# Performance work log

Hardware: AMD Instinct MI355X
Metric: run time of the kernel (lower is better)

Reference implementation:

```python
import jax, jax.numpy as jnp
import numpy as np

N_NODES = 50000
N_EDGES = 800000
N_GRAPHS = 128
IN_CH, HIDDEN, OUT_CH = 16, 64, 2


def gcn_conv(x, src, dst, W, b, n_nodes):
    """GCNConv: add self-loops, sym-normalized adjacency scatter-add, linear."""
    h = x @ W  # [N, H]
    loop = jnp.arange(n_nodes, dtype=src.dtype)
    s = jnp.concatenate([src, loop])  # [E+N]
    d = jnp.concatenate([dst, loop])
    deg = jax.ops.segment_sum(jnp.ones_like(d, dtype=h.dtype), d, num_segments=n_nodes)
    dinv = jnp.where(deg > 0, jax.lax.rsqrt(deg), 0.0)  # deg^{-1/2}
    norm = dinv[s] * dinv[d]  # [E+N]
    msg = h[s] * norm[:, None]  # gather + scale, [E+N, H]
    out = jax.ops.segment_sum(msg, d, num_segments=n_nodes)  # scatter-add
    return out + b


def global_mean_pool(x, batch, n_graphs):
    sums = jax.ops.segment_sum(x, batch, num_segments=n_graphs)
    cnts = jax.ops.segment_sum(jnp.ones((x.shape[0],), x.dtype), batch, num_segments=n_graphs)
    return sums / jnp.maximum(cnts, 1.0)[:, None]


def setup_inputs() -> dict:
    key = jax.random.key(0)
    ks = jax.random.split(key, 10)
    x = jax.random.normal(ks[0], (N_NODES, IN_CH), dtype=jnp.float32)
    edge_index = jax.random.randint(ks[1], (2, N_EDGES), 0, N_NODES, dtype=jnp.int64)
    batch = jnp.sort(jax.random.randint(ks[2], (N_NODES,), 0, N_GRAPHS, dtype=jnp.int64))
    def glorot(k, shp):
        lim = float(np.sqrt(6.0 / (shp[0] + shp[1])))
        return jax.random.uniform(k, shp, jnp.float32, -lim, lim)
    W1 = glorot(ks[3], (IN_CH, HIDDEN))
    b1 = jnp.zeros((HIDDEN,), jnp.float32)
    W2 = glorot(ks[4], (HIDDEN, HIDDEN))
    b2 = jnp.zeros((HIDDEN,), jnp.float32)
    Wc = glorot(ks[5], (HIDDEN, OUT_CH))
    bc = jnp.zeros((OUT_CH,), jnp.float32)
    return {"x": x, "edge_index": edge_index, "batch": batch,
            "W1": W1, "b1": b1, "W2": W2, "b2": b2, "Wc": Wc, "bc": bc}


def reference(x, edge_index, batch, W1, b1, W2, b2, Wc, bc):
    src, dst = edge_index[0], edge_index[1]
    n = x.shape[0]
    h = jax.nn.relu(gcn_conv(x, src, dst, W1, b1, n))
    # dropout p=0.3 is identity in eval mode
    h = jax.nn.relu(gcn_conv(h, src, dst, W2, b2, n))
    g = global_mean_pool(h, batch, N_GRAPHS)  # [G, H]
    return g @ Wc + bc  # [G, out_channels]
```

## Files before the change

kernel.cpp:

```cpp
#include <hip/hip_runtime.h>
#include <hip/hip_bf16.h>

#define N_NODES 50000
#define N_EDGES 800000
#define N_GRAPHS 128
#define IN_CH 16
#define HIDDEN 64
#define OUT_CH 2

#define BSHIFT 7
#define BNODES 128
#define NB ((N_NODES + BNODES - 1) / BNODES)
#define ECHUNK 4096
#define EB ((N_EDGES + ECHUNK - 1) / ECHUNK)
#define SLEN (NB * EB)
#define SCHUNK 1024
#define NSB ((SLEN + SCHUNK - 1) / SCHUNK)
#define MAXK 12
#define WT1_LD 18
#define AGG_LD 72
#define W2T_ENT (HIDDEN * AGG_LD)

typedef __attribute__((ext_vector_type(8))) short bf16x8;
typedef __attribute__((ext_vector_type(4))) float f32x4;

__device__ __forceinline__ float bf2f(unsigned short u) {
    return __uint_as_float(((unsigned)u) << 16);
}
__device__ __forceinline__ unsigned short f2bf(float f) {
    __hip_bfloat16 h = __float2bfloat16(f);
    return *reinterpret_cast<unsigned short*>(&h);
}


__global__ void bucket_hist_kernel(const int* __restrict__ dst, int* __restrict__ bh,
                                   float* __restrict__ sums, float* __restrict__ cntg,
                                   const float* __restrict__ W2, unsigned short* __restrict__ w2t) {
    __shared__ int lh[NB];
    int t = threadIdx.x;
    if (blockIdx.x == 0) {
        for (int i = t; i < N_GRAPHS * HIDDEN; i += 256) sums[i] = 0.0f;
        if (t < N_GRAPHS) cntg[t] = 0.0f;
    }
    if (blockIdx.x == 1) {
        for (int i = t; i < HIDDEN * HIDDEN; i += 256) {
            int k = i >> 6, c = i & 63;
            w2t[c * AGG_LD + k] = f2bf(W2[i]);
        }
    }
    for (int i = t; i < NB; i += 256) lh[i] = 0;
    __syncthreads();
    int base = blockIdx.x * ECHUNK;
    for (int i = t; i < ECHUNK; i += 256) {
        int e = base + i;
        if (e < N_EDGES) {
            int d = dst[e];
            if ((unsigned)d < N_NODES) atomicAdd(&lh[d >> BSHIFT], 1);
        }
    }
    __syncthreads();
    for (int i = t; i < NB; i += 256) bh[i * EB + blockIdx.x] = lh[i];
}

__global__ void scan_part_kernel(const int* __restrict__ a, int* __restrict__ bsum) {
    __shared__ int s[256];
    int t = threadIdx.x;
    int ebase = blockIdx.x * SCHUNK + t * 4;
    int v = 0;
    if (ebase + 3 < SLEN) {
        int4 c = *(const int4*)&a[ebase];
        v = c.x + c.y + c.z + c.w;
    } else {
        for (int k = 0; k < 4; k++) {
            int i = ebase + k;
            if (i < SLEN) v += a[i];
        }
    }
    s[t] = v;
    __syncthreads();
    for (int off = 128; off > 0; off >>= 1) {
        if (t < off) s[t] += s[t + off];
        __syncthreads();
    }
    if (t == 0) bsum[blockIdx.x] = s[0];
}

__global__ void scan_apply_kernel(const int* __restrict__ a, const int* __restrict__ bsum,
                                  int* __restrict__ boff) {
    __shared__ int sb[256];
    __shared__ int st[256];
    int t = threadIdx.x;
    sb[t] = (t < NSB) ? bsum[t] : 0;
    __syncthreads();
    for (int off = 1; off < 256; off <<= 1) {
        int u = (t >= off) ? sb[t - off] : 0;
        __syncthreads();
        sb[t] += u;
        __syncthreads();
    }
    int blockOff = (blockIdx.x > 0) ? sb[blockIdx.x - 1] : 0;

    int ebase = blockIdx.x * SCHUNK + t * 4;
    int c0 = 0, c1 = 0, c2 = 0, c3 = 0;
    bool full = (ebase + 3 < SLEN);
    if (full) {
        int4 c = *(const int4*)&a[ebase];
        c0 = c.x; c1 = c.y; c2 = c.z; c3 = c.w;
    } else {
        if (ebase < SLEN) c0 = a[ebase];
        if (ebase + 1 < SLEN) c1 = a[ebase + 1];
        if (ebase + 2 < SLEN) c2 = a[ebase + 2];
    }
    int tsum = c0 + c1 + c2 + c3;
    st[t] = tsum;
    __syncthreads();
    for (int off = 1; off < 256; off <<= 1) {
        int u = (t >= off) ? st[t - off] : 0;
        __syncthreads();
        st[t] += u;
        __syncthreads();
    }
    int p = blockOff + st[t] - tsum;
    if (full) {
        int4 o;
        o.x = p; o.y = p + c0; o.z = p + c0 + c1; o.w = p + c0 + c1 + c2;
        *(int4*)&boff[ebase] = o;
    } else {
        if (ebase < SLEN) boff[ebase] = p;
        if (ebase + 1 < SLEN) boff[ebase + 1] = p + c0;
        if (ebase + 2 < SLEN) boff[ebase + 2] = p + c0 + c1;
        if (ebase + 3 < SLEN) boff[ebase + 3] = p + c0 + c1 + c2;
    }
}

__global__ void bucket_scatter_kernel(const int* __restrict__ src, const int* __restrict__ dst,
                                      const int* __restrict__ boff, int* __restrict__ pairs) {
    __shared__ int lcnt[NB];
    __shared__ int goff[NB];
    int t = threadIdx.x;
    for (int i = t; i < NB; i += 256) {
        lcnt[i] = 0;
        goff[i] = boff[i * EB + blockIdx.x];
    }
    __syncthreads();
    int base = blockIdx.x * ECHUNK;
    for (int i = t; i < ECHUNK; i += 256) {
        int e = base + i;
        if (e < N_EDGES) {
            int d = dst[e];
            if ((unsigned)d < N_NODES) {
                int b = d >> BSHIFT;
                int r = atomicAdd(&lcnt[b], 1);
                pairs[goff[b] + r] = (src[e] << BSHIFT) | (d & (BNODES - 1));
            }
        }
    }
}

__global__ void bucket_csr_kernel(const int* __restrict__ pairs, const int* __restrict__ boff,
                                  int* __restrict__ csr, int* __restrict__ rowptr,
                                  int* __restrict__ cnt_node, float* __restrict__ dinv) {
    __shared__ int lcnt[BNODES];
    __shared__ int ls[BNODES];
    __shared__ int lrow[BNODES];
    int b = blockIdx.x;
    int t = threadIdx.x;
    if (t < BNODES) lcnt[t] = 0;
    __syncthreads();
    int bstart = boff[b * EB];
    int bend = (b + 1 < NB) ? boff[(b + 1) * EB] : N_EDGES;
    int K = bend - bstart;
    int myp[MAXK], myr[MAXK];
#pragma unroll
    for (int k = 0; k < MAXK; k++) {
        int i = k * 256 + t;
        if (i < K) {
            int p = pairs[bstart + i];
            myp[k] = p;
            myr[k] = atomicAdd(&lcnt[p & (BNODES - 1)], 1);
        }
    }
    __syncthreads();
    if (t < BNODES) ls[t] = lcnt[t];
    __syncthreads();
    for (int off = 1; off < BNODES; off <<= 1) {
        int u = (t >= off && t < BNODES) ? ls[t - off] : 0;
        __syncthreads();
        if (t < BNODES) ls[t] += u;
        __syncthreads();
    }
    if (t < BNODES) {
        int ex = ls[t] - lcnt[t];
        lrow[t] = ex;
        int n = b * BNODES + t;
        if (n < N_NODES) {
            rowptr[n] = bstart + ex;
            cnt_node[n] = lcnt[t];
            dinv[n] = rsqrtf((float)(lcnt[t] + 1));
        }
    }
    __syncthreads();
#pragma unroll
    for (int k = 0; k < MAXK; k++) {
        int i = k * 256 + t;
        if (i < K) csr[bstart + lrow[myp[k] & (BNODES - 1)] + myr[k]] = myp[k] >> BSHIFT;
    }
}


__global__ void fused_l1_kernel(const float* __restrict__ x, const int* __restrict__ csr_src,
                                const int* __restrict__ rowptr, const int* __restrict__ cnt,
                                const float* __restrict__ dinv, const float* __restrict__ W,
                                const float* __restrict__ b, __hip_bfloat16* __restrict__ h) {
    __shared__ float sWT[HIDDEN * WT1_LD];
    __shared__ float sx[16 * IN_CH];
    int t = threadIdx.x;
    for (int i = t; i < IN_CH * HIDDEN; i += 256) {
        int k = i >> 6, c = i & 63;
        sWT[c * WT1_LD + k] = W[i];
    }

    int n0 = blockIdx.x * 16;
    int w = t >> 6;
    int lane = t & 63;
    int e16 = lane >> 2;
    int cc = (lane & 3) * 4;

    int lens[4], starts[4];
#pragma unroll
    for (int q = 0; q < 4; q++) {
        int n = n0 + w * 4 + q;
        lens[q] = cnt[n];
        starts[q] = rowptr[n];
    }

    for (int q = 0; q < 4; q++) {
        int row = w * 4 + q;
        int n = n0 + row;
        int len = lens[q];
        int start = starts[q];
        float4 acc = make_float4(0.f, 0.f, 0.f, 0.f);
        for (int i = e16; i < len; i += 16) {
            int s = csr_src[start + i];
            float dv = dinv[s];
            float4 xv = *(const float4*)&x[s * IN_CH + cc];
            acc.x += dv * xv.x; acc.y += dv * xv.y;
            acc.z += dv * xv.z; acc.w += dv * xv.w;
        }
#pragma unroll
        for (int m = 4; m <= 32; m <<= 1) {
            acc.x += __shfl_xor(acc.x, m, 64);
            acc.y += __shfl_xor(acc.y, m, 64);
            acc.z += __shfl_xor(acc.z, m, 64);
            acc.w += __shfl_xor(acc.w, m, 64);
        }
        if (lane < 4) {
            float dn = dinv[n];
            float4 xs = *(const float4*)&x[n * IN_CH + cc];
            float4 v;
            v.x = dn * acc.x + dn * dn * xs.x;
            v.y = dn * acc.y + dn * dn * xs.y;
            v.z = dn * acc.z + dn * dn * xs.z;
            v.w = dn * acc.w + dn * dn * xs.w;
            *(float4*)&sx[row * IN_CH + cc] = v;
        }
    }
    __syncthreads();

    int r = w;
    int c = t & 63;
    float bias = b[c];
#pragma unroll
    for (int nb = 0; nb < 4; nb++) {
        int row = nb * 4 + r;
        int n = n0 + row;
        if (n >= N_NODES) continue;
        float acch = bias;
#pragma unroll
        for (int k4 = 0; k4 < IN_CH; k4 += 4) {
            float4 a = *(const float4*)&sx[row * IN_CH + k4];
            float2 w0 = *(const float2*)&sWT[c * WT1_LD + k4];
            float2 w1 = *(const float2*)&sWT[c * WT1_LD + k4 + 2];
            acch += a.x * w0.x + a.y * w0.y + a.z * w1.x + a.w * w1.y;
        }
        float v = acch > 0.0f ? acch : 0.0f;
        h[n * HIDDEN + c] = __float2bfloat16(dinv[n] * v);
    }
}


__global__ void fused_l2_kernel(const __hip_bfloat16* __restrict__ h, const int* __restrict__ csr_src,
                                const int* __restrict__ rowptr, const int* __restrict__ cnt,
                                const float* __restrict__ dinv, const unsigned short* __restrict__ w2t,
                                const float* __restrict__ b, const int* __restrict__ batch,
                                float* __restrict__ sums, float* __restrict__ cntg) {
    __shared__ unsigned short sW[W2T_ENT];
    __shared__ unsigned short sagg[16 * AGG_LD];
    int t = threadIdx.x;
    {
        const uint4* wp = (const uint4*)w2t;
        uint4* sWv = (uint4*)sW;
#pragma unroll
        for (int i = 0; i < 3; i++) {
            int idx = i * 256 + t;
            if (idx < W2T_ENT / 8) sWv[idx] = wp[idx];
        }
    }

    int n0 = blockIdx.x * 16;
    int w = t >> 6;
    int lane = t & 63;
    int e4 = lane >> 4;
    int cc = (lane & 15) * 4;
    const unsigned short* hu = (const unsigned short*)h;

    int lens[4], starts[4];
#pragma unroll
    for (int q = 0; q < 4; q++) {
        int n = n0 + w * 4 + q;
        lens[q] = cnt[n];
        starts[q] = rowptr[n];
    }

    for (int q = 0; q < 4; q++) {
        int row = w * 4 + q;
        int n = n0 + row;
        int len = lens[q];
        int start = starts[q];
        float4 acc = make_float4(0.f, 0.f, 0.f, 0.f);
        int last = len - 1;
        int iters = (len + 15) >> 4;
        for (int m = 0; m < iters; m++) {
            int base = m * 16 + e4;
#pragma unroll
            for (int k = 0; k < 4; k++) {
                int j = base + 4 * k;
                int jj = j <= last ? j : last;
                float msk = j <= last ? 1.0f : 0.0f;
                int s = csr_src[start + jj];
                ushort4 a = *(const ushort4*)&hu[s * HIDDEN + cc];
                acc.x += msk * bf2f(a.x);
                acc.y += msk * bf2f(a.y);
                acc.z += msk * bf2f(a.z);
                acc.w += msk * bf2f(a.w);
            }
        }
        acc.x += __shfl_xor(acc.x, 16, 64);
        acc.y += __shfl_xor(acc.y, 16, 64);
        acc.z += __shfl_xor(acc.z, 16, 64);
        acc.w += __shfl_xor(acc.w, 16, 64);
        acc.x += __shfl_xor(acc.x, 32, 64);
        acc.y += __shfl_xor(acc.y, 32, 64);
        acc.z += __shfl_xor(acc.z, 32, 64);
        acc.w += __shfl_xor(acc.w, 32, 64);
        if (lane < 16) {
            ushort4 sv = *(const ushort4*)&hu[n * HIDDEN + cc];
            float dn = dinv[n];
            ushort4 o;
            o.x = f2bf(dn * (acc.x + bf2f(sv.x)));
            o.y = f2bf(dn * (acc.y + bf2f(sv.y)));
            o.z = f2bf(dn * (acc.z + bf2f(sv.z)));
            o.w = f2bf(dn * (acc.w + bf2f(sv.w)));
            *(ushort4*)&sagg[row * AGG_LD + cc] = o;
        }
    }
    __syncthreads();

    int quad = lane >> 4;
    int col = lane & 15;
    int cch = w * 16 + col;
    bf16x8 a0 = *(const bf16x8*)&sagg[col * AGG_LD + quad * 8];
    bf16x8 a1 = *(const bf16x8*)&sagg[col * AGG_LD + 32 + quad * 8];
    bf16x8 b0 = *(const bf16x8*)&sW[cch * AGG_LD + quad * 8];
    bf16x8 b1 = *(const bf16x8*)&sW[cch * AGG_LD + 32 + quad * 8];
    f32x4 d = {0.f, 0.f, 0.f, 0.f};
    d = __builtin_amdgcn_mfma_f32_16x16x32_bf16(a0, b0, d, 0, 0, 0);
    d = __builtin_amdgcn_mfma_f32_16x16x32_bf16(a1, b1, d, 0, 0, 0);
    float bias = b[cch];
    float v[4];
#pragma unroll
    for (int r = 0; r < 4; r++) {
        float z = d[r] + bias;
        v[r] = z > 0.0f ? z : 0.0f;
    }

    int glo = batch[n0];
    int ghi = batch[n0 + 15];
    if (glo == ghi) {
        float s4 = (v[0] + v[1]) + (v[2] + v[3]);
        s4 += __shfl_xor(s4, 16, 64);
        s4 += __shfl_xor(s4, 32, 64);
        if (quad == 0) atomicAdd(&sums[glo * HIDDEN + cch], s4);
        if (t == 0) atomicAdd(&cntg[glo], 16.0f);
    } else {
#pragma unroll
        for (int r = 0; r < 4; r++) {
            int g = batch[n0 + quad * 4 + r];
            if ((unsigned)g < N_GRAPHS) atomicAdd(&sums[g * HIDDEN + cch], v[r]);
        }
        if (w == 0 && col == 0) {
#pragma unroll
            for (int r = 0; r < 4; r++) {
                int g = batch[n0 + quad * 4 + r];
                if ((unsigned)g < N_GRAPHS) atomicAdd(&cntg[g], 1.0f);
            }
        }
    }
}


__global__ void head_kernel(const float* __restrict__ sums, const float* __restrict__ cntg,
                            const float* __restrict__ Wc, const float* __restrict__ bc,
                            float* __restrict__ out) {
    int t = blockIdx.x * blockDim.x + threadIdx.x;
    if (t >= N_GRAPHS * OUT_CH) return;
    int g = t >> 1;
    int o = t & 1;
    float inv = 1.0f / fmaxf(cntg[g], 1.0f);
    float acc = bc[o];
#pragma unroll
    for (int k = 0; k < HIDDEN; k++) acc += sums[g * HIDDEN + k] * inv * Wc[k * OUT_CH + o];
    out[t] = acc;
}


extern "C" void kernel_launch(void* const* d_in, const int* in_sizes, int n_in,
                              void* d_out, int out_size, void* d_ws, size_t ws_size,
                              hipStream_t stream) {
    const float* x  = (const float*)d_in[0];
    const int* ei   = (const int*)d_in[1];
    const int* bat  = (const int*)d_in[2];
    const float* W1 = (const float*)d_in[3];
    const float* b1 = (const float*)d_in[4];
    const float* W2 = (const float*)d_in[5];
    const float* b2 = (const float*)d_in[6];
    const float* Wc = (const float*)d_in[7];
    const float* bc = (const float*)d_in[8];
    float* out = (float*)d_out;

    const int* src = ei;
    const int* dst = ei + N_EDGES;

    char* ws = (char*)d_ws;
    size_t off = 0;
    auto carve = [&](size_t nbytes) {
        char* p = ws + off;
        off += (nbytes + 255) & ~(size_t)255;
        return p;
    };
    float* sums     = (float*)carve(N_GRAPHS * HIDDEN * sizeof(float));
    float* cntg     = (float*)carve(N_GRAPHS * sizeof(float));
    unsigned short* w2t = (unsigned short*)carve(W2T_ENT * sizeof(unsigned short));
    int*   bh       = (int*)carve((size_t)SLEN * sizeof(int));
    int*   bsum     = (int*)carve(NSB * sizeof(int));
    int*   boff     = (int*)carve((size_t)SLEN * sizeof(int));
    int*   pairs    = (int*)carve((size_t)N_EDGES * sizeof(int));
    int*   csr      = (int*)carve((size_t)N_EDGES * sizeof(int));
    int*   rowptr   = (int*)carve(N_NODES * sizeof(int));
    int*   cnt_node = (int*)carve(N_NODES * sizeof(int));
    float* dinv     = (float*)carve(N_NODES * sizeof(float));
    __hip_bfloat16* bufA = (__hip_bfloat16*)carve((size_t)N_NODES * HIDDEN * sizeof(__hip_bfloat16));
    (void)ws_size;

    const int node16Blk = (N_NODES + 15) / 16;

    bucket_hist_kernel<<<EB, 256, 0, stream>>>(dst, bh, sums, cntg, W2, w2t);
    scan_part_kernel<<<NSB, 256, 0, stream>>>(bh, bsum);
    scan_apply_kernel<<<NSB, 256, 0, stream>>>(bh, bsum, boff);
    bucket_scatter_kernel<<<EB, 256, 0, stream>>>(src, dst, boff, pairs);
    bucket_csr_kernel<<<NB, 256, 0, stream>>>(pairs, boff, csr, rowptr, cnt_node, dinv);

    fused_l1_kernel<<<node16Blk, 256, 0, stream>>>(x, csr, rowptr, cnt_node, dinv, W1, b1, bufA);
    fused_l2_kernel<<<node16Blk, 256, 0, stream>>>(bufA, csr, rowptr, cnt_node, dinv, w2t, b2,
                                                   bat, sums, cntg);
    head_kernel<<<1, 256, 0, stream>>>(sums, cntg, Wc, bc, out);
}
```

Measured before the change: 171.9 us.

## Replace scan-based bucketing with fixed-capacity atomic buckets and prescaled features

Drops the histogram and two scan kernels. Edges are now placed into fixed-capacity per-bucket slots (BCAP), with offsets claimed through global atomics in the scatter kernel. The CSR kernel also writes x prescaled by dinv, so layer 1 skips the per-edge dinv gather and unrolls its gather two-wide. Layer 2's gather switches to 8 bf16 per lane with 16-byte loads. Edges beyond BCAP in a bucket are silently dropped, and edge order within a bucket becomes nondeterministic.

```diff
diff --git a/kernel.cpp b/kernel.cpp
--- a/kernel.cpp
+++ b/kernel.cpp
@@ -11,11 +11,9 @@
 #define BSHIFT 7
 #define BNODES 128
 #define NB ((N_NODES + BNODES - 1) / BNODES)
+#define BCAP 3072
 #define ECHUNK 4096
 #define EB ((N_EDGES + ECHUNK - 1) / ECHUNK)
-#define SLEN (NB * EB)
-#define SCHUNK 1024
-#define NSB ((SLEN + SCHUNK - 1) / SCHUNK)
 #define MAXK 12
 #define WT1_LD 18
 #define AGG_LD 72
@@ -33,143 +31,69 @@
 }
 
 
-__global__ void bucket_hist_kernel(const int* __restrict__ dst, int* __restrict__ bh,
-                                   float* __restrict__ sums, float* __restrict__ cntg,
-                                   const float* __restrict__ W2, unsigned short* __restrict__ w2t) {
-    __shared__ int lh[NB];
+__global__ void init_kernel(int* __restrict__ zbase, int zwords,
+                            const float* __restrict__ W2, unsigned short* __restrict__ w2t) {
+    int gid = blockIdx.x * 256 + threadIdx.x;
+    int gsz = gridDim.x * 256;
+    for (int i = gid; i < zwords; i += gsz) zbase[i] = 0;
+    for (int i = gid; i < HIDDEN * HIDDEN; i += gsz) {
+        int k = i >> 6, c = i & 63;
+        w2t[c * AGG_LD + k] = f2bf(W2[i]);
+    }
+}
+
+
+__global__ void bucket_scatter_kernel(const int* __restrict__ src, const int* __restrict__ dst,
+                                      int* __restrict__ bcnt, int* __restrict__ pairs) {
+    __shared__ int lcnt[NB];
+    __shared__ int goff[NB];
+    __shared__ int lcur[NB];
     int t = threadIdx.x;
-    if (blockIdx.x == 0) {
-        for (int i = t; i < N_GRAPHS * HIDDEN; i += 256) sums[i] = 0.0f;
-        if (t < N_GRAPHS) cntg[t] = 0.0f;
-    }
-    if (blockIdx.x == 1) {
-        for (int i = t; i < HIDDEN * HIDDEN; i += 256) {
-            int k = i >> 6, c = i & 63;
-            w2t[c * AGG_LD + k] = f2bf(W2[i]);
-        }
-    }
-    for (int i = t; i < NB; i += 256) lh[i] = 0;
+    for (int i = t; i < NB; i += 256) lcnt[i] = 0;
     __syncthreads();
     int base = blockIdx.x * ECHUNK;
     for (int i = t; i < ECHUNK; i += 256) {
         int e = base + i;
         if (e < N_EDGES) {
             int d = dst[e];
-            if ((unsigned)d < N_NODES) atomicAdd(&lh[d >> BSHIFT], 1);
-        }
-    }
-    __syncthreads();
-    for (int i = t; i < NB; i += 256) bh[i * EB + blockIdx.x] = lh[i];
-}
-
-__global__ void scan_part_kernel(const int* __restrict__ a, int* __restrict__ bsum) {
-    __shared__ int s[256];
-    int t = threadIdx.x;
-    int ebase = blockIdx.x * SCHUNK + t * 4;
-    int v = 0;
-    if (ebase + 3 < SLEN) {
-        int4 c = *(const int4*)&a[ebase];
-        v = c.x + c.y + c.z + c.w;
-    } else {
-        for (int k = 0; k < 4; k++) {
-            int i = ebase + k;
-            if (i < SLEN) v += a[i];
-        }
-    }
-    s[t] = v;
-    __syncthreads();
-    for (int off = 128; off > 0; off >>= 1) {
-        if (t < off) s[t] += s[t + off];
-        __syncthreads();
-    }
-    if (t == 0) bsum[blockIdx.x] = s[0];
-}
-
-__global__ void scan_apply_kernel(const int* __restrict__ a, const int* __restrict__ bsum,
-                                  int* __restrict__ boff) {
-    __shared__ int sb[256];
-    __shared__ int st[256];
-    int t = threadIdx.x;
-    sb[t] = (t < NSB) ? bsum[t] : 0;
-    __syncthreads();
-    for (int off = 1; off < 256; off <<= 1) {
-        int u = (t >= off) ? sb[t - off] : 0;
-        __syncthreads();
-        sb[t] += u;
-        __syncthreads();
-    }
-    int blockOff = (blockIdx.x > 0) ? sb[blockIdx.x - 1] : 0;
-
-    int ebase = blockIdx.x * SCHUNK + t * 4;
-    int c0 = 0, c1 = 0, c2 = 0, c3 = 0;
-    bool full = (ebase + 3 < SLEN);
-    if (full) {
-        int4 c = *(const int4*)&a[ebase];
-        c0 = c.x; c1 = c.y; c2 = c.z; c3 = c.w;
-    } else {
-        if (ebase < SLEN) c0 = a[ebase];
-        if (ebase + 1 < SLEN) c1 = a[ebase + 1];
-        if (ebase + 2 < SLEN) c2 = a[ebase + 2];
-    }
-    int tsum = c0 + c1 + c2 + c3;
-    st[t] = tsum;
-    __syncthreads();
-    for (int off = 1; off < 256; off <<= 1) {
-        int u = (t >= off) ? st[t - off] : 0;
-        __syncthreads();
-        st[t] += u;
-        __syncthreads();
-    }
-    int p = blockOff + st[t] - tsum;
-    if (full) {
-        int4 o;
-        o.x = p; o.y = p + c0; o.z = p + c0 + c1; o.w = p + c0 + c1 + c2;
-        *(int4*)&boff[ebase] = o;
-    } else {
-        if (ebase < SLEN) boff[ebase] = p;
-        if (ebase + 1 < SLEN) boff[ebase + 1] = p + c0;
-        if (ebase + 2 < SLEN) boff[ebase + 2] = p + c0 + c1;
-        if (ebase + 3 < SLEN) boff[ebase + 3] = p + c0 + c1 + c2;
-    }
-}
-
-__global__ void bucket_scatter_kernel(const int* __restrict__ src, const int* __restrict__ dst,
-                                      const int* __restrict__ boff, int* __restrict__ pairs) {
-    __shared__ int lcnt[NB];
-    __shared__ int goff[NB];
-    int t = threadIdx.x;
+            if ((unsigned)d < N_NODES) atomicAdd(&lcnt[d >> BSHIFT], 1);
+        }
+    }
+    __syncthreads();
     for (int i = t; i < NB; i += 256) {
-        lcnt[i] = 0;
-        goff[i] = boff[i * EB + blockIdx.x];
-    }
-    __syncthreads();
-    int base = blockIdx.x * ECHUNK;
+        int c = lcnt[i];
+        goff[i] = (c > 0) ? atomicAdd(&bcnt[i], c) : 0;
+        lcur[i] = 0;
+    }
+    __syncthreads();
     for (int i = t; i < ECHUNK; i += 256) {
         int e = base + i;
         if (e < N_EDGES) {
             int d = dst[e];
             if ((unsigned)d < N_NODES) {
                 int b = d >> BSHIFT;
-                int r = atomicAdd(&lcnt[b], 1);
-                pairs[goff[b] + r] = (src[e] << BSHIFT) | (d & (BNODES - 1));
+                int r = goff[b] + atomicAdd(&lcur[b], 1);
+                if (r < BCAP) pairs[b * BCAP + r] = (src[e] << BSHIFT) | (d & (BNODES - 1));
             }
         }
     }
 }
 
-__global__ void bucket_csr_kernel(const int* __restrict__ pairs, const int* __restrict__ boff,
+__global__ void bucket_csr_kernel(const int* __restrict__ pairs, const int* __restrict__ bcnt,
                                   int* __restrict__ csr, int* __restrict__ rowptr,
-                                  int* __restrict__ cnt_node, float* __restrict__ dinv) {
+                                  int* __restrict__ cnt_node, float* __restrict__ dinv,
+                                  const float* __restrict__ x, float* __restrict__ xs) {
     __shared__ int lcnt[BNODES];
     __shared__ int ls[BNODES];
     __shared__ int lrow[BNODES];
+    __shared__ float sdv[BNODES];
     int b = blockIdx.x;
     int t = threadIdx.x;
     if (t < BNODES) lcnt[t] = 0;
     __syncthreads();
-    int bstart = boff[b * EB];
-    int bend = (b + 1 < NB) ? boff[(b + 1) * EB] : N_EDGES;
-    int K = bend - bstart;
+    int bstart = b * BCAP;
+    int K = bcnt[b];
+    if (K > BCAP) K = BCAP;
     int myp[MAXK], myr[MAXK];
 #pragma unroll
     for (int k = 0; k < MAXK; k++) {
@@ -192,11 +116,13 @@
     if (t < BNODES) {
         int ex = ls[t] - lcnt[t];
         lrow[t] = ex;
+        float dv = rsqrtf((float)(lcnt[t] + 1));
+        sdv[t] = dv;
         int n = b * BNODES + t;
         if (n < N_NODES) {
             rowptr[n] = bstart + ex;
             cnt_node[n] = lcnt[t];
-            dinv[n] = rsqrtf((float)(lcnt[t] + 1));
+            dinv[n] = dv;
         }
     }
     __syncthreads();
@@ -205,10 +131,15 @@
         int i = k * 256 + t;
         if (i < K) csr[bstart + lrow[myp[k] & (BNODES - 1)] + myr[k]] = myp[k] >> BSHIFT;
     }
-}
-
-
-__global__ void fused_l1_kernel(const float* __restrict__ x, const int* __restrict__ csr_src,
+    for (int i = t; i < BNODES * IN_CH; i += 256) {
+        int nl = i >> 4;
+        int n = b * BNODES + nl;
+        if (n < N_NODES) xs[n * IN_CH + (i & 15)] = sdv[nl] * x[n * IN_CH + (i & 15)];
+    }
+}
+
+
+__global__ void fused_l1_kernel(const float* __restrict__ xs, const int* __restrict__ csr_src,
                                 const int* __restrict__ rowptr, const int* __restrict__ cnt,
                                 const float* __restrict__ dinv, const float* __restrict__ W,
                                 const float* __restrict__ b, __hip_bfloat16* __restrict__ h) {
@@ -239,13 +170,21 @@
         int n = n0 + row;
         int len = lens[q];
         int start = starts[q];
+        int last = len - 1;
+        int iters = (len + 31) >> 5;
         float4 acc = make_float4(0.f, 0.f, 0.f, 0.f);
-        for (int i = e16; i < len; i += 16) {
-            int s = csr_src[start + i];
-            float dv = dinv[s];
-            float4 xv = *(const float4*)&x[s * IN_CH + cc];
-            acc.x += dv * xv.x; acc.y += dv * xv.y;
-            acc.z += dv * xv.z; acc.w += dv * xv.w;
+        for (int m = 0; m < iters; m++) {
+            int base = m * 32 + e16;
+#pragma unroll
+            for (int k = 0; k < 2; k++) {
+                int j = base + 16 * k;
+                int jj = j <= last ? j : last;
+                float msk = j <= last ? 1.0f : 0.0f;
+                int s = csr_src[start + jj];
+                float4 xv = *(const float4*)&xs[s * IN_CH + cc];
+                acc.x += msk * xv.x; acc.y += msk * xv.y;
+                acc.z += msk * xv.z; acc.w += msk * xv.w;
+            }
         }
 #pragma unroll
         for (int m = 4; m <= 32; m <<= 1) {
@@ -256,12 +195,12 @@
         }
         if (lane < 4) {
             float dn = dinv[n];
-            float4 xs = *(const float4*)&x[n * IN_CH + cc];
+            float4 xsv = *(const float4*)&xs[n * IN_CH + cc];
             float4 v;
-            v.x = dn * acc.x + dn * dn * xs.x;
-            v.y = dn * acc.y + dn * dn * xs.y;
-            v.z = dn * acc.z + dn * dn * xs.z;
-            v.w = dn * acc.w + dn * dn * xs.w;
+            v.x = dn * (acc.x + xsv.x);
+            v.y = dn * (acc.y + xsv.y);
+            v.z = dn * (acc.z + xsv.z);
+            v.w = dn * (acc.w + xsv.w);
             *(float4*)&sx[row * IN_CH + cc] = v;
         }
     }
@@ -310,8 +249,8 @@
     int n0 = blockIdx.x * 16;
     int w = t >> 6;
     int lane = t & 63;
-    int e4 = lane >> 4;
-    int cc = (lane & 15) * 4;
+    int e8 = lane >> 3;
+    int cc8 = (lane & 7) * 8;
     const unsigned short* hu = (const unsigned short*)h;
 
     int lens[4], starts[4];
@@ -327,41 +266,54 @@
         int n = n0 + row;
         int len = lens[q];
         int start = starts[q];
-        float4 acc = make_float4(0.f, 0.f, 0.f, 0.f);
         int last = len - 1;
-        int iters = (len + 15) >> 4;
+        int iters = (len + 31) >> 5;
+        float4 alo = make_float4(0.f, 0.f, 0.f, 0.f);
+        float4 ahi = make_float4(0.f, 0.f, 0.f, 0.f);
         for (int m = 0; m < iters; m++) {
-            int base = m * 16 + e4;
+            int base = m * 32 + e8;
 #pragma unroll
             for (int k = 0; k < 4; k++) {
-                int j = base + 4 * k;
+                int j = base + 8 * k;
                 int jj = j <= last ? j : last;
                 float msk = j <= last ? 1.0f : 0.0f;
                 int s = csr_src[start + jj];
-                ushort4 a = *(const ushort4*)&hu[s * HIDDEN + cc];
-                acc.x += msk * bf2f(a.x);
-                acc.y += msk * bf2f(a.y);
-                acc.z += msk * bf2f(a.z);
-                acc.w += msk * bf2f(a.w);
+                uint4 raw = *(const uint4*)&hu[s * HIDDEN + cc8];
+                alo.x += msk * __uint_as_float(raw.x << 16);
+                alo.y += msk * __uint_as_float(raw.x & 0xffff0000u);
+                alo.z += msk * __uint_as_float(raw.y << 16);
+                alo.w += msk * __uint_as_float(raw.y & 0xffff0000u);
+                ahi.x += msk * __uint_as_float(raw.z << 16);
+                ahi.y += msk * __uint_as_float(raw.z & 0xffff0000u);
+                ahi.z += msk * __uint_as_float(raw.w << 16);
+                ahi.w += msk * __uint_as_float(raw.w & 0xffff0000u);
             }
         }
-        acc.x += __shfl_xor(acc.x, 16, 64);
-        acc.y += __shfl_xor(acc.y, 16, 64);
-        acc.z += __shfl_xor(acc.z, 16, 64);
-        acc.w += __shfl_xor(acc.w, 16, 64);
-        acc.x += __shfl_xor(acc.x, 32, 64);
-        acc.y += __shfl_xor(acc.y, 32, 64);
-        acc.z += __shfl_xor(acc.z, 32, 64);
-        acc.w += __shfl_xor(acc.w, 32, 64);
-        if (lane < 16) {
-            ushort4 sv = *(const ushort4*)&hu[n * HIDDEN + cc];
+#pragma unroll
+        for (int m = 8; m <= 32; m <<= 1) {
+            alo.x += __shfl_xor(alo.x, m, 64);
+            alo.y += __shfl_xor(alo.y, m, 64);
+            alo.z += __shfl_xor(alo.z, m, 64);
+            alo.w += __shfl_xor(alo.w, m, 64);
+            ahi.x += __shfl_xor(ahi.x, m, 64);
+            ahi.y += __shfl_xor(ahi.y, m, 64);
+            ahi.z += __shfl_xor(ahi.z, m, 64);
+            ahi.w += __shfl_xor(ahi.w, m, 64);
+        }
+        if (lane < 8) {
+            uint4 sv = *(const uint4*)&hu[n * HIDDEN + cc8];
             float dn = dinv[n];
-            ushort4 o;
-            o.x = f2bf(dn * (acc.x + bf2f(sv.x)));
-            o.y = f2bf(dn * (acc.y + bf2f(sv.y)));
-            o.z = f2bf(dn * (acc.z + bf2f(sv.z)));
-            o.w = f2bf(dn * (acc.w + bf2f(sv.w)));
-            *(ushort4*)&sagg[row * AGG_LD + cc] = o;
+            ushort4 o0, o1;
+            o0.x = f2bf(dn * (alo.x + __uint_as_float(sv.x << 16)));
+            o0.y = f2bf(dn * (alo.y + __uint_as_float(sv.x & 0xffff0000u)));
+            o0.z = f2bf(dn * (alo.z + __uint_as_float(sv.y << 16)));
+            o0.w = f2bf(dn * (alo.w + __uint_as_float(sv.y & 0xffff0000u)));
+            o1.x = f2bf(dn * (ahi.x + __uint_as_float(sv.z << 16)));
+            o1.y = f2bf(dn * (ahi.y + __uint_as_float(sv.z & 0xffff0000u)));
+            o1.z = f2bf(dn * (ahi.z + __uint_as_float(sv.w << 16)));
+            o1.w = f2bf(dn * (ahi.w + __uint_as_float(sv.w & 0xffff0000u)));
+            *(ushort4*)&sagg[row * AGG_LD + cc8] = o0;
+            *(ushort4*)&sagg[row * AGG_LD + cc8 + 4] = o1;
         }
     }
     __syncthreads();
@@ -450,27 +402,25 @@
     };
     float* sums     = (float*)carve(N_GRAPHS * HIDDEN * sizeof(float));
     float* cntg     = (float*)carve(N_GRAPHS * sizeof(float));
+    int*   bcnt     = (int*)carve(NB * sizeof(int));
+    size_t zeroBytes = off;
     unsigned short* w2t = (unsigned short*)carve(W2T_ENT * sizeof(unsigned short));
-    int*   bh       = (int*)carve((size_t)SLEN * sizeof(int));
-    int*   bsum     = (int*)carve(NSB * sizeof(int));
-    int*   boff     = (int*)carve((size_t)SLEN * sizeof(int));
-    int*   pairs    = (int*)carve((size_t)N_EDGES * sizeof(int));
-    int*   csr      = (int*)carve((size_t)N_EDGES * sizeof(int));
+    int*   pairs    = (int*)carve((size_t)NB * BCAP * sizeof(int));
+    int*   csr      = (int*)carve((size_t)NB * BCAP * sizeof(int));
     int*   rowptr   = (int*)carve(N_NODES * sizeof(int));
     int*   cnt_node = (int*)carve(N_NODES * sizeof(int));
     float* dinv     = (float*)carve(N_NODES * sizeof(float));
+    float* xs       = (float*)carve((size_t)N_NODES * IN_CH * sizeof(float));
     __hip_bfloat16* bufA = (__hip_bfloat16*)carve((size_t)N_NODES * HIDDEN * sizeof(__hip_bfloat16));
     (void)ws_size;
 
     const int node16Blk = (N_NODES + 15) / 16;
 
-    bucket_hist_kernel<<<EB, 256, 0, stream>>>(dst, bh, sums, cntg, W2, w2t);
-    scan_part_kernel<<<NSB, 256, 0, stream>>>(bh, bsum);
-    scan_apply_kernel<<<NSB, 256, 0, stream>>>(bh, bsum, boff);
-    bucket_scatter_kernel<<<EB, 256, 0, stream>>>(src, dst, boff, pairs);
-    bucket_csr_kernel<<<NB, 256, 0, stream>>>(pairs, boff, csr, rowptr, cnt_node, dinv);
-
-    fused_l1_kernel<<<node16Blk, 256, 0, stream>>>(x, csr, rowptr, cnt_node, dinv, W1, b1, bufA);
+    init_kernel<<<32, 256, 0, stream>>>((int*)sums, (int)(zeroBytes / 4), W2, w2t);
+    bucket_scatter_kernel<<<EB, 256, 0, stream>>>(src, dst, bcnt, pairs);
+    bucket_csr_kernel<<<NB, 256, 0, stream>>>(pairs, bcnt, csr, rowptr, cnt_node, dinv, x, xs);
+
+    fused_l1_kernel<<<node16Blk, 256, 0, stream>>>(xs, csr, rowptr, cnt_node, dinv, W1, b1, bufA);
     fused_l2_kernel<<<node16Blk, 256, 0, stream>>>(bufA, csr, rowptr, cnt_node, dinv, w2t, b2,
                                                    bat, sums, cntg);
     head_kernel<<<1, 256, 0, stream>>>(sums, cntg, Wc, bc, out);
```

New measurement: 167.6 us. 1.03x faster.
